# Kernel tuning notes

Measured on AMD Instinct MI355X. Metric: run time of the kernel, lower is better.

The kernel has to match this reference:

```python
import jax, jax.numpy as jnp
import numpy as np

N_NODES = 4096
N_EDGES = 16384
L = 512
MP_STEPS = 5
DT = 0.01


def _mlp(x, W1, b1, W2, b2):
    return jax.nn.relu(x @ W1 + b1) @ W2 + b2


def _ln(x):
    m = jnp.mean(x, axis=-1, keepdims=True)
    v = jnp.var(x, axis=-1, keepdims=True)
    return (x - m) * jax.lax.rsqrt(v + 1e-6)


_PARAM_SHAPES = [
    ("enc_e_W1", (1, L)), ("enc_e_b1", (L,)), ("enc_e_W2", (L, L)), ("enc_e_b2", (L,)),
    ("enc_n_W1", (1, L)), ("enc_n_b1", (L,)), ("enc_n_W2", (L, L)), ("enc_n_b2", (L,)),
    ("proc_e_W1", (3 * L, L)), ("proc_e_b1", (L,)), ("proc_e_W2", (L, L)), ("proc_e_b2", (L,)),
    ("proc_n_W1", (2 * L, L)), ("proc_n_b1", (L,)), ("proc_n_W2", (L, L)), ("proc_n_b2", (L,)),
    ("dec_e_W1", (L, L)), ("dec_e_b1", (L,)), ("dec_e_W2", (L, 1)), ("dec_e_b2", (1,)),
]


def setup_inputs() -> dict:
    key = jax.random.key(0)
    ks = jax.random.split(key, 3 + len(_PARAM_SHAPES))
    d = {}
    d["state"] = jax.random.normal(ks[0], (N_EDGES + N_NODES,), dtype=jnp.float32)
    d["senders"] = jax.random.randint(ks[1], (N_EDGES,), 0, N_NODES)
    d["receivers"] = jax.random.randint(ks[2], (N_EDGES,), 0, N_NODES)
    for i, (name, shp) in enumerate(_PARAM_SHAPES):
        if name.endswith(("b1", "b2")):
            d[name] = jnp.zeros(shp, dtype=jnp.float32)
        else:
            d[name] = 0.02 * jax.random.normal(ks[3 + i], shp, dtype=jnp.float32)
    return d


def _hamiltonian(x, senders, receivers,
                 enc_e_W1, enc_e_b1, enc_e_W2, enc_e_b2,
                 enc_n_W1, enc_n_b1, enc_n_W2, enc_n_b2,
                 proc_e_W1, proc_e_b1, proc_e_W2, proc_e_b2,
                 proc_n_W1, proc_n_b1, proc_n_W2, proc_n_b2,
                 dec_e_W1, dec_e_b1, dec_e_W2, dec_e_b2):
    # graph_from_state: edge scalars then node scalars
    e = x[:N_EDGES].reshape(N_EDGES, 1)
    n = x[N_EDGES:].reshape(N_NODES, 1)
    # encode (MLP + layer norm)
    eh = _ln(_mlp(e, enc_e_W1, enc_e_b1, enc_e_W2, enc_e_b2))  # [E, L]
    nh = _ln(_mlp(n, enc_n_W1, enc_n_b1, enc_n_W2, enc_n_b2))  # [N, L]
    # process: num_mp_steps of GraphNetwork-style message passing, shared params
    for _ in range(MP_STEPS):
        msg_in = jnp.concatenate([eh, nh[senders], nh[receivers]], axis=-1)  # [E, 3L]
        eh = eh + _mlp(msg_in, proc_e_W1, proc_e_b1, proc_e_W2, proc_e_b2)
        agg = jax.ops.segment_sum(eh, receivers, num_segments=N_NODES)  # [N, L]
        node_in = jnp.concatenate([nh, agg], axis=-1)  # [N, 2L]
        nh = nh + _mlp(node_in, proc_n_W1, proc_n_b1, proc_n_W2, proc_n_b2)
    # decode edges to scalars; H = sum of decoded edge energies
    dec_e = _mlp(eh, dec_e_W1, dec_e_b1, dec_e_W2, dec_e_b2)  # [E, 1]
    return jnp.sum(dec_e)


def reference(state, senders, receivers,
              enc_e_W1, enc_e_b1, enc_e_W2, enc_e_b2,
              enc_n_W1, enc_n_b1, enc_n_W2, enc_n_b2,
              proc_e_W1, proc_e_b1, proc_e_W2, proc_e_b2,
              proc_n_W1, proc_n_b1, proc_n_W2, proc_n_b2,
              dec_e_W1, dec_e_b1, dec_e_W2, dec_e_b2):
    def H_fn(x):
        return _hamiltonian(x, senders, receivers,
                            enc_e_W1, enc_e_b1, enc_e_W2, enc_e_b2,
                            enc_n_W1, enc_n_b1, enc_n_W2, enc_n_b2,
                            proc_e_W1, proc_e_b1, proc_e_W2, proc_e_b2,
                            proc_n_W1, proc_n_b1, proc_n_W2, proc_n_b2,
                            dec_e_W1, dec_e_b1, dec_e_W2, dec_e_b2)
    H, dH = jax.value_and_grad(H_fn)(state)
    # one integrator step driven by the Hamiltonian gradient (stand-in for DAE solve)
    next_state = state - DT * dH
    return next_state
```

## Files before the change

kernel.cpp:

```cpp
#include <hip/hip_runtime.h>


#define E_ROWS 16384
#define N_ROWS 4096
#define ALL_ROWS 20480
#define DT_F   0.01f

typedef unsigned char u8;
typedef unsigned short u16;
typedef unsigned long long u64;
typedef __attribute__((ext_vector_type(8))) short short8v;
typedef __attribute__((ext_vector_type(4))) float f32x4;

__device__ __forceinline__ u16 f2b(float f) {
    union { float f; unsigned u; } v; v.f = f;
    unsigned r = v.u + 0x7FFF + ((v.u >> 16) & 1);
    return (u16)(r >> 16);
}
__device__ __forceinline__ float b2f(u16 u) {
    union { unsigned u; float f; } v; v.u = ((unsigned)u) << 16;
    return v.f;
}

template<int BM, int WM, int WN, int KTOT, int LDA, int LDC,
         bool ADD_C, bool GATHER2, bool BIAS, bool RELU_MASK, bool APPLY_MASK,
         bool WF32, bool WBF16, bool DUALOUT, bool ROWDOT, bool DECW2, bool BSEL>
__global__ __launch_bounds__(256)
void bgemm(const u16* __restrict__ A, const u16* __restrict__ Bt, const u16* __restrict__ Bt2,
           float* __restrict__ C, u16* __restrict__ Cb,
           const u16* __restrict__ Cinb, const float* __restrict__ bias,
           const float* __restrict__ bias2, const u16* __restrict__ G12b,
           const int* __restrict__ sidx, const int* __restrict__ ridx,
           u8* __restrict__ maskw, u16* __restrict__ C2b,
           const float* __restrict__ wvec, const float* __restrict__ wvec2,
           float* __restrict__ outp)
{
    constexpr int BN = WN * 64;
    constexpr int NA = BM / 16;
    constexpr int TC = (BM + BN) / 16;
    constexpr int PER = TC / 4;
    constexpr int IFRAG = BM / WM / 16;
    __shared__ u16 Ls[BM * BN];

    const int tid = threadIdx.x;
    const int lane = tid & 63;
    const int wv = tid >> 6;
    const int wr = wv / WN;
    const int wc = wv % WN;

    const int gx = gridDim.x;
    int id = blockIdx.y * gx + blockIdx.x;
    const int nwg = gx * gridDim.y;
    id = (id & 7) * (nwg >> 3) + (id >> 3);
    const int bx = id % gx;
    const int by = id / gx;
    const int rowBase = by * BM;
    const int colBase = bx * BN;

    const u16* BtU = Bt;
    const float* biasU = bias;
    const float* wvecU = wvec;
    if (BSEL && rowBase >= E_ROWS) { BtU = Bt2; biasU = bias2; wvecU = wvec2; }

    const int srow = lane & 15;
    const int slotk = (lane >> 4) << 3;

    const u16* srcs[PER];
    int dstoff[PER];
#pragma unroll
    for (int q = 0; q < PER; ++q) {
        const int c = wv + (q << 2);
        if (c < NA)
            srcs[q] = A + (size_t)(rowBase + c * 16 + srow) * LDA + slotk;
        else
            srcs[q] = BtU + (size_t)(colBase + (c - NA) * 16 + srow) * KTOT + slotk;
        dstoff[q] = c * 512;
    }

    f32x4 acc[IFRAG][4];
#pragma unroll
    for (int i = 0; i < IFRAG; ++i)
#pragma unroll
        for (int j = 0; j < 4; ++j)
            acc[i][j] = (f32x4){0.f, 0.f, 0.f, 0.f};

    const int fro = ((lane >> 4) << 7) + ((lane & 15) << 3);

    for (int kb = 0; kb < KTOT; kb += 32) {
#pragma unroll
        for (int q = 0; q < PER; ++q)
            __builtin_amdgcn_global_load_lds(
                (const __attribute__((address_space(1))) void*)(srcs[q] + kb),
                (__attribute__((address_space(3))) void*)&Ls[dstoff[q]], 16, 0, 0);
        __syncthreads();
        short8v af[IFRAG], bfm[4];
#pragma unroll
        for (int i = 0; i < IFRAG; ++i)
            af[i] = *(const short8v*)&Ls[((wr * IFRAG + i) << 9) + fro];
#pragma unroll
        for (int j = 0; j < 4; ++j)
            bfm[j] = *(const short8v*)&Ls[((NA + (wc << 2) + j) << 9) + fro];
#pragma unroll
        for (int i = 0; i < IFRAG; ++i)
#pragma unroll
            for (int j = 0; j < 4; ++j)
                acc[i][j] = __builtin_amdgcn_mfma_f32_16x16x32_bf16(af[i], bfm[j], acc[i][j], 0, 0, 0);
        __syncthreads();
    }

    if constexpr (WF32) {
        const int colB = colBase + wc * 64 + (lane & 15);
        const int rowB = rowBase + wr * (BM / WM) + ((lane >> 4) << 2);
        float bcol[4];
#pragma unroll
        for (int j = 0; j < 4; ++j) bcol[j] = biasU[colB + (j << 4)];
#pragma unroll
        for (int i = 0; i < IFRAG; ++i)
#pragma unroll
            for (int r = 0; r < 4; ++r) {
                const int row = rowB + (i << 4) + r;
#pragma unroll
                for (int j = 0; j < 4; ++j)
                    C[(size_t)row * LDC + colB + (j << 4)] = acc[i][j][r] + bcol[j];
            }
    } else {
        const int colL = wc * 64 + (lane & 15);
        const int rowL0 = wr * (BM / WM) + ((lane >> 4) << 2);
#pragma unroll
        for (int i = 0; i < IFRAG; ++i)
#pragma unroll
            for (int r = 0; r < 4; ++r) {
                const int row = rowL0 + (i << 4) + r;
#pragma unroll
                for (int j = 0; j < 4; ++j) {
                    const int col = colL + (j << 4);
                    int byte = row * (BN * 2) + col * 2;
                    byte ^= (row & 7) << 4;
                    *(u16*)((char*)Ls + byte) = f2b(acc[i][j][r]);
                }
            }
        __syncthreads();

        constexpr int TPR = BN / 8;
        constexpr int RPP = 256 / TPR;
        constexpr int NP = BM / RPP;
        const int rloc = tid / TPR;
        const int seg = tid % TPR;
        const int col0 = seg * 8;
        const bool upper = DUALOUT && (colBase >= 512);
#pragma unroll
        for (int p = 0; p < NP; ++p) {
            const int row = p * RPP + rloc;
            const int grow = rowBase + row;
            const int gcol = colBase + col0;
            int byte = row * (BN * 2) + col0 * 2;
            byte ^= (row & 7) << 4;
            const short8v sv = *(const short8v*)((const char*)Ls + byte);
            float v[8];
#pragma unroll
            for (int e = 0; e < 8; ++e) v[e] = b2f((u16)sv[e]);

            if (DUALOUT && upper) {
                short8v res;
#pragma unroll
                for (int e = 0; e < 8; ++e) res[e] = (short)f2b(v[e]);
                *(short8v*)&C2b[(size_t)grow * 512 + (gcol - 512)] = res;
                continue;
            }
            if (GATHER2) {
                const int si = sidx[grow], ri = ridx[grow];
                const short8v g1 = *(const short8v*)&G12b[(size_t)si * 1024 + gcol];
                const short8v g2 = *(const short8v*)&G12b[(size_t)ri * 1024 + 512 + gcol];
#pragma unroll
                for (int e = 0; e < 8; ++e) v[e] += b2f((u16)g1[e]) + b2f((u16)g2[e]);
            }
            if (ADD_C) {
                const short8v c8 = *(const short8v*)&Cinb[(size_t)grow * LDC + gcol];
#pragma unroll
                for (int e = 0; e < 8; ++e) v[e] += b2f((u16)c8[e]);
            }
            if (BIAS) {
                const float4 b0 = *(const float4*)&biasU[gcol];
                const float4 b1 = *(const float4*)&biasU[gcol + 4];
                v[0] += b0.x; v[1] += b0.y; v[2] += b0.z; v[3] += b0.w;
                v[4] += b1.x; v[5] += b1.y; v[6] += b1.z; v[7] += b1.w;
            }
            if (DECW2) {
                const float4 w0 = *(const float4*)&wvecU[gcol];
                const float4 w1 = *(const float4*)&wvecU[gcol + 4];
                const float wl[8] = {w0.x, w0.y, w0.z, w0.w, w1.x, w1.y, w1.z, w1.w};
                short8v res;
#pragma unroll
                for (int e = 0; e < 8; ++e) res[e] = (v[e] > 0.f) ? (short)f2b(wl[e]) : (short)0;
                *(short8v*)&Cb[(size_t)grow * LDC + gcol] = res;
                continue;
            }
            if (RELU_MASK) {
                u64 mm = 0;
#pragma unroll
                for (int e = 0; e < 8; ++e) {
                    const bool m = v[e] > 0.f;
                    mm |= (u64)(m ? 1 : 0) << (e * 8);
                    if (!m) v[e] = 0.f;
                }
                *(u64*)&maskw[(size_t)grow * 512 + gcol] = mm;
            }
            if (APPLY_MASK) {
                const u64 mm = *(const u64*)&maskw[(size_t)grow * 512 + gcol];
#pragma unroll
                for (int e = 0; e < 8; ++e)
                    if (!((mm >> (e * 8)) & 0xff)) v[e] = 0.f;
            }
            if (ROWDOT) {
                const float4 w0 = *(const float4*)&wvecU[gcol];
                const float4 w1 = *(const float4*)&wvecU[gcol + 4];
                float rds = v[0] * w0.x + v[1] * w0.y + v[2] * w0.z + v[3] * w0.w
                          + v[4] * w1.x + v[5] * w1.y + v[6] * w1.z + v[7] * w1.w;
#pragma unroll
                for (int m = 1; m < TPR; m <<= 1) rds += __shfl_xor(rds, m);
                if (seg == 0) atomicAdd(outp + grow, -DT_F * rds);
            }
            if (WBF16) {
                short8v res;
#pragma unroll
                for (int e = 0; e < 8; ++e) res[e] = (short)f2b(v[e]);
                *(short8v*)&Cb[(size_t)grow * LDC + gcol] = res;
            }
        }
    }
}

struct WArgs {
    const float* src[10];
    u16* dstP[10];
    u16* dstT[10];
    int ldP[10], ldT[10];
};

__global__ void wcvt_kernel(WArgs a)
{
    const int i = blockIdx.z;
    const float* W = a.src[i];
    u16* P = a.dstP[i]; const int lp = a.ldP[i];
    u16* T = a.dstT[i]; const int lt = a.ldT[i];
    __shared__ u16 t[64][66];
    const int rb = blockIdx.y << 6, cb = blockIdx.x << 6;
    const int tr = threadIdx.x >> 4;
    const int tc = (threadIdx.x & 15) << 2;
#pragma unroll
    for (int rr = 0; rr < 4; ++rr) {
        const int r = tr + (rr << 4);
        const float4 v = *(const float4*)&W[(size_t)(rb + r) * 512 + cb + tc];
        ushort4 u; u.x = f2b(v.x); u.y = f2b(v.y); u.z = f2b(v.z); u.w = f2b(v.w);
        *(ushort4*)&P[(size_t)(rb + r) * lp + cb + tc] = u;
        t[r][tc] = u.x; t[r][tc + 1] = u.y; t[r][tc + 2] = u.z; t[r][tc + 3] = u.w;
    }
    __syncthreads();
#pragma unroll
    for (int rr = 0; rr < 4; ++rr) {
        const int n = tr + (rr << 4);
        ushort4 u;
        u.x = t[tc][n]; u.y = t[tc + 1][n]; u.z = t[tc + 2][n]; u.w = t[tc + 3][n];
        *(ushort4*)&T[(size_t)(cb + n) * lt + rb + tc] = u;
    }
}

__device__ void csr_build(const int* __restrict__ idx, int* __restrict__ starts,
                          int* __restrict__ eids)
{
    __shared__ int hist[4096];
    __shared__ int scanbuf[1024];
    const int t = threadIdx.x;
    for (int i = t; i < 4096; i += 1024) hist[i] = 0;
    __syncthreads();
    for (int e = t; e < 16384; e += 1024) atomicAdd(&hist[idx[e]], 1);
    __syncthreads();
    const int base = t << 2;
    const int l0 = hist[base], l1 = hist[base + 1], l2 = hist[base + 2], l3 = hist[base + 3];
    const int lsum = l0 + l1 + l2 + l3;
    scanbuf[t] = lsum;
    __syncthreads();
    for (int ofs = 1; ofs < 1024; ofs <<= 1) {
        const int v = scanbuf[t];
        const int u = (t >= ofs) ? scanbuf[t - ofs] : 0;
        __syncthreads();
        scanbuf[t] = v + u;
        __syncthreads();
    }
    const int excl = scanbuf[t] - lsum;
    const int p0 = excl, p1 = p0 + l0, p2 = p1 + l1, p3 = p2 + l2;
    starts[base] = p0; starts[base + 1] = p1; starts[base + 2] = p2; starts[base + 3] = p3;
    if (t == 0) starts[4096] = 16384;
    __syncthreads();
    hist[base] = p0; hist[base + 1] = p1; hist[base + 2] = p2; hist[base + 3] = p3;
    __syncthreads();
    for (int e = t; e < 16384; e += 1024) {
        const int pos = atomicAdd(&hist[idx[e]], 1);
        eids[pos] = e;
    }
    __syncthreads();
    for (int n = t; n < 4096; n += 1024) {
        const int s0 = starts[n], s1 = hist[n];
        for (int i = s0 + 1; i < s1; ++i) {
            const int v = eids[i];
            int j = i - 1;
            while (j >= s0 && eids[j] > v) { eids[j + 1] = eids[j]; --j; }
            eids[j + 1] = v;
        }
    }
}

__global__ __launch_bounds__(1024) void csr2_kernel(const int* __restrict__ senders,
                                                    const int* __restrict__ receivers,
                                                    int* __restrict__ sst, int* __restrict__ seid,
                                                    int* __restrict__ rst, int* __restrict__ reid)
{
    if (blockIdx.x == 0) csr_build(receivers, rst, reid);
    else                 csr_build(senders, sst, seid);
}

__global__ void init_out_kernel(const float* __restrict__ state, float* __restrict__ out)
{
    const int t = blockIdx.x * 256 + threadIdx.x;
    out[t] = state[t];
}

__global__ void seg_agg_fwd_kernel(const u16* __restrict__ ehb, const int* __restrict__ starts,
                                   const int* __restrict__ eids, const u16* __restrict__ nhb,
                                   u16* __restrict__ nagg)
{
    const int n = blockIdx.x, c = threadIdx.x;
    const int s0 = starts[n], s1 = starts[n + 1];
    float a0 = 0.f, a1 = 0.f;
    for (int i = s0; i < s1; ++i) {
        const u16* p = ehb + (size_t)eids[i] * 512;
        a0 += b2f(p[c]); a1 += b2f(p[c + 256]);
    }
    u16* d = nagg + (size_t)n * 1024;
    const u16* s = nhb + (size_t)n * 512;
    d[c] = s[c]; d[c + 256] = s[c + 256];
    d[512 + c] = f2b(a0); d[768 + c] = f2b(a1);
}

__global__ void seg_sr_bwd_kernel(const u16* __restrict__ dh1e,
                                  const int* __restrict__ sst, const int* __restrict__ seid,
                                  const int* __restrict__ rst, const int* __restrict__ reid,
                                  u16* __restrict__ SR)
{
    const int n = blockIdx.x, c = threadIdx.x;
    float a0 = 0.f, a1 = 0.f, b0 = 0.f, b1 = 0.f;
    for (int i = sst[n]; i < sst[n + 1]; ++i) {
        const u16* p = dh1e + (size_t)seid[i] * 512;
        a0 += b2f(p[c]); a1 += b2f(p[c + 256]);
    }
    for (int i = rst[n]; i < rst[n + 1]; ++i) {
        const u16* p = dh1e + (size_t)reid[i] * 512;
        b0 += b2f(p[c]); b1 += b2f(p[c + 256]);
    }
    u16* d = SR + (size_t)n * 1024;
    d[c] = f2b(a0); d[c + 256] = f2b(a1);
    d[512 + c] = f2b(b0); d[768 + c] = f2b(b1);
}

__global__ void enc_h1_kernel(const float* __restrict__ x,
                              const float* __restrict__ W1e, const float* __restrict__ b1e,
                              const float* __restrict__ W1n, const float* __restrict__ b1n,
                              u16* __restrict__ h1b, u8* __restrict__ mask)
{
    const int idx = blockIdx.x * 256 + threadIdx.x;
    const int row = idx >> 7;
    const int c = (idx & 127) << 2;
    const bool edge = row < E_ROWS;
    const float* W1 = edge ? W1e : W1n;
    const float* b1 = edge ? b1e : b1n;
    const float xv = x[row];
    const float4 w = *(const float4*)&W1[c];
    const float4 b = *(const float4*)&b1[c];
    float4 v;
    v.x = fmaf(xv, w.x, b.x); v.y = fmaf(xv, w.y, b.y);
    v.z = fmaf(xv, w.z, b.z); v.w = fmaf(xv, w.w, b.w);
    uchar4 m;
    m.x = v.x > 0.f; m.y = v.y > 0.f; m.z = v.z > 0.f; m.w = v.w > 0.f;
    v.x = m.x ? v.x : 0.f; v.y = m.y ? v.y : 0.f;
    v.z = m.z ? v.z : 0.f; v.w = m.w ? v.w : 0.f;
    const size_t o = (size_t)row * 512 + c;
    ushort4 u; u.x = f2b(v.x); u.y = f2b(v.y); u.z = f2b(v.z); u.w = f2b(v.w);
    *(ushort4*)&h1b[o] = u;
    *(uchar4*)&mask[o] = m;
}

__global__ void ln_fwd_kernel(const float* __restrict__ x, u16* __restrict__ xhat_b,
                              u16* __restrict__ xb, float* __restrict__ rstd_save)
{
    const int row = blockIdx.x, tid = threadIdx.x;
    const float* p = x + (size_t)row * 512;
    const float a = p[tid], b = p[tid + 256];
    __shared__ float s1[256], s2[256];
    s1[tid] = a + b; s2[tid] = a * a + b * b;
    __syncthreads();
    for (int d = 128; d > 0; d >>= 1) {
        if (tid < d) { s1[tid] += s1[tid + d]; s2[tid] += s2[tid + d]; }
        __syncthreads();
    }
    const float mean = s1[0] * (1.f / 512.f);
    const float var = s2[0] * (1.f / 512.f) - mean * mean;
    const float r = rsqrtf(var + 1e-6f);
    const float ya = (a - mean) * r, yb = (b - mean) * r;
    const size_t o = (size_t)row * 512 + tid;
    xhat_b[o] = f2b(ya); xhat_b[o + 256] = f2b(yb);
    xb[o] = f2b(ya); xb[o + 256] = f2b(yb);
    if (tid == 0) rstd_save[row] = r;
}

__global__ void ln_bwd_kernel(u16* __restrict__ d, const u16* __restrict__ xhat_b,
                              const float* __restrict__ rstd)
{
    const int row = blockIdx.x, tid = threadIdx.x;
    u16* p = d + (size_t)row * 512;
    const u16* xh = xhat_b + (size_t)row * 512;
    const float da = b2f(p[tid]), dbv = b2f(p[tid + 256]);
    const float xa = b2f(xh[tid]), xbv = b2f(xh[tid + 256]);
    __shared__ float s1[256], s2[256];
    s1[tid] = da + dbv; s2[tid] = da * xa + dbv * xbv;
    __syncthreads();
    for (int dd = 128; dd > 0; dd >>= 1) {
        if (tid < dd) { s1[tid] += s1[tid + dd]; s2[tid] += s2[tid + dd]; }
        __syncthreads();
    }
    const float m1 = s1[0] * (1.f / 512.f);
    const float m2 = s2[0] * (1.f / 512.f);
    const float r = rstd[row];
    p[tid] = f2b(r * (da - m1 - xa * m2));
    p[tid + 256] = f2b(r * (dbv - m1 - xbv * m2));
}

__global__ void gather_add_kernel(u16* __restrict__ dst, const u16* __restrict__ src,
                                  const int* __restrict__ idx)
{
    const int t = blockIdx.x * 256 + threadIdx.x;
    const int row = t >> 6;
    const int c = (t & 63) << 3;
    const size_t o = (size_t)row * 512 + c;
    short8v a = *(const short8v*)&dst[o];
    const short8v g = *(const short8v*)&src[(size_t)idx[row] * 512 + c];
    short8v r;
#pragma unroll
    for (int i = 0; i < 8; ++i)
        r[i] = (short)f2b(b2f((u16)a[i]) + b2f((u16)g[i]));
    *(short8v*)&dst[o] = r;
}

extern "C" void kernel_launch(void* const* d_in, const int* in_sizes, int n_in,
                              void* d_out, int out_size, void* d_ws, size_t ws_size,
                              hipStream_t stream)
{
    (void)in_sizes; (void)n_in; (void)out_size; (void)ws_size;
    const float* state     = (const float*)d_in[0];
    const int*   senders   = (const int*)d_in[1];
    const int*   receivers = (const int*)d_in[2];
    const float* enc_e_W1 = (const float*)d_in[3];
    const float* enc_e_b1 = (const float*)d_in[4];
    const float* enc_e_W2 = (const float*)d_in[5];
    const float* enc_e_b2 = (const float*)d_in[6];
    const float* enc_n_W1 = (const float*)d_in[7];
    const float* enc_n_b1 = (const float*)d_in[8];
    const float* enc_n_W2 = (const float*)d_in[9];
    const float* enc_n_b2 = (const float*)d_in[10];
    const float* pe_W1 = (const float*)d_in[11];
    const float* pe_b1 = (const float*)d_in[12];
    const float* pe_W2 = (const float*)d_in[13];
    const float* pe_b2 = (const float*)d_in[14];
    const float* pn_W1 = (const float*)d_in[15];
    const float* pn_b1 = (const float*)d_in[16];
    const float* pn_W2 = (const float*)d_in[17];
    const float* pn_b2 = (const float*)d_in[18];
    const float* de_W1 = (const float*)d_in[19];
    const float* de_b1 = (const float*)d_in[20];
    const float* de_W2 = (const float*)d_in[21];
    float* out = (float*)d_out;

    const size_t EL = (size_t)E_ROWS * 512, NL = (size_t)N_ROWS * 512;
    const size_t AL = (size_t)ALL_ROWS * 512;
    const size_t LL = 512 * 512;
    char* w = (char*)d_ws;
    size_t off = 0;
    auto carve = [&](size_t bytes) -> char* {
        char* p = w + off;
        off += (bytes + 255) & ~(size_t)255;
        return p;
    };
    u16* wb = (u16*)carve(20 * LL * 2);
    u16* WT0 = wb;           u16* WT1 = wb + LL;      u16* WT2 = wb + 2 * LL;
    u16* WT34 = wb + 3 * LL;                          u16* WT5 = wb + 5 * LL;
    u16* WT8 = wb + 6 * LL;  u16* WT9 = wb + 7 * LL;
    u16* WP0 = wb + 8 * LL;  u16* WP1 = wb + 9 * LL;  u16* WP2 = wb + 10 * LL;
    u16* WP5 = wb + 11 * LL; u16* WP8 = wb + 12 * LL; u16* WP9 = wb + 13 * LL;
    u16* WT67 = wb + 14 * LL;
    u16* WP34c = wb + 16 * LL;
    u16* WP67 = wb + 18 * LL;

    float* eh  = (float*)carve(AL * 4);
    u16* ehb   = (u16*)carve(EL * 2);
    u16* nhb   = (u16*)carve(NL * 2);
    u16* h1eb  = (u16*)carve(EL * 2);
    u16* h1nb  = (u16*)carve(NL * 2);
    u16* eh0b  = (u16*)carve(EL * 2);
    u16* nh0b  = (u16*)carve(NL * 2);
    u8* menc   = (u8*)carve(AL);
    u16* G1b   = (u16*)carve(NL * 2);
    u16* G12b  = (u16*)carve(NL * 2 * 2);
    u16* nsr   = (u16*)carve(NL * 2 * 2);
    float* rstd = (float*)carve(ALL_ROWS * 4);
    u8* mpe    = (u8*)carve(5 * EL);
    u8* mpn    = (u8*)carve(5 * NL);
    int* rst  = (int*)carve(4097 * 4);
    int* reid = (int*)carve(16384 * 4);
    int* sst  = (int*)carve(4097 * 4);
    int* seid = (int*)carve(16384 * 4);

    const dim3 blk(256);
    const dim3 gE(4, E_ROWS / 128);
    const dim3 gA(4, ALL_ROWS / 128);
    const dim3 gN512(8, N_ROWS / 64);
    const dim3 gN1024(16, N_ROWS / 64);
    const float* fp = nullptr;
    u16* up = nullptr;
    const u16* cup = nullptr;
    const int* ip = nullptr;
    u8* mp = nullptr;
    float* f2p = nullptr;

    WArgs wa;
    const float* wsrc[10] = { enc_e_W2, enc_n_W2, pe_W1, pe_W1 + LL, pe_W1 + 2 * LL,
                              pe_W2, pn_W1, pn_W1 + LL, pn_W2, de_W1 };
    u16* dstP[10] = { WP0, WP1, WP2, WP34c, WP34c + 512, WP5, WP67, WP67 + LL, WP8, WP9 };
    int  ldP [10] = { 512, 512, 512, 1024,  1024,        512, 512,  512,       512, 512 };
    u16* dstT[10] = { WT0, WT1, WT2, WT34, WT34 + LL, WT5, WT67, WT67 + 512, WT8, WT9 };
    int  ldT [10] = { 512, 512, 512, 512,  512,       512, 1024, 1024,       512, 512 };
    for (int i = 0; i < 10; ++i) {
        wa.src[i] = wsrc[i]; wa.dstP[i] = dstP[i]; wa.dstT[i] = dstT[i];
        wa.ldP[i] = ldP[i]; wa.ldT[i] = ldT[i];
    }
    wcvt_kernel<<<dim3(8, 8, 10), blk, 0, stream>>>(wa);

    csr2_kernel<<<2, 1024, 0, stream>>>(senders, receivers, sst, seid, rst, reid);
    init_out_kernel<<<ALL_ROWS / 256, blk, 0, stream>>>(state, out);

    enc_h1_kernel<<<ALL_ROWS * 128 / 256, blk, 0, stream>>>(state, enc_e_W1, enc_e_b1,
                                                            enc_n_W1, enc_n_b1, h1eb, menc);
    bgemm<128,2,2,512,512,512, false,false,true,false,false, true,false,false,false,false,true>
        <<<gA, blk, 0, stream>>>(h1eb, WT0, WT1, eh, up, cup, enc_e_b2, enc_n_b2, cup, ip, ip, mp, up, fp, fp, f2p);
    ln_fwd_kernel<<<ALL_ROWS, blk, 0, stream>>>(eh, eh0b, ehb, rstd);

    for (int k = 0; k < 5; ++k) {
        bgemm<64,4,1,512,512,1024, false,false,false,false,false, false,true,false,false,false,false>
            <<<gN1024, blk, 0, stream>>>(nhb, WT34, cup, f2p, G12b, cup, fp, fp, cup, ip, ip, mp, up, fp, fp, f2p);
        bgemm<128,2,2,512,512,512, false,true,true,true,false, false,true,false,false,false,false>
            <<<gE, blk, 0, stream>>>(ehb, WT2, cup, f2p, h1eb, cup, pe_b1, fp, G12b, senders, receivers, mpe + (size_t)k * EL, up, fp, fp, f2p);
        bgemm<128,2,2,512,512,512, true,false,true,false,false, false,true,false,false,false,false>
            <<<gE, blk, 0, stream>>>(h1eb, WT5, cup, f2p, ehb, ehb, pe_b2, fp, cup, ip, ip, mp, up, fp, fp, f2p);
        seg_agg_fwd_kernel<<<N_ROWS, blk, 0, stream>>>(ehb, rst, reid, nhb, nsr);
        bgemm<64,4,1,1024,1024,512, false,false,true,true,false, false,true,false,false,false,false>
            <<<gN512, blk, 0, stream>>>(nsr, WT67, cup, f2p, h1nb, cup, pn_b1, fp, cup, ip, ip, mpn + (size_t)k * NL, up, fp, fp, f2p);
        bgemm<64,4,1,512,512,512, true,false,true,false,false, false,true,false,false,false,false>
            <<<gN512, blk, 0, stream>>>(h1nb, WT8, cup, f2p, nhb, nhb, pn_b2, fp, cup, ip, ip, mp, up, fp, fp, f2p);
    }

    bgemm<128,2,2,512,512,512, false,false,true,false,false, false,false,false,false,true,false>
        <<<gE, blk, 0, stream>>>(ehb, WT9, cup, f2p, h1eb, cup, de_b1, fp, cup, ip, ip, mp, up, de_W2, fp, f2p);

    bgemm<128,2,2,512,512,512, false,false,false,false,false, false,true,false,false,false,false>
        <<<gE, blk, 0, stream>>>(h1eb, WP9, cup, f2p, ehb, cup, fp, fp, cup, ip, ip, mp, up, fp, fp, f2p);

    for (int k = 4; k >= 0; --k) {
        if (k < 4) {
            bgemm<64,4,1,512,512,512, false,false,false,false,true, false,true,false,false,false,false>
                <<<gN512, blk, 0, stream>>>(nhb, WP8, cup, f2p, h1nb, cup, fp, fp, cup, ip, ip, mpn + (size_t)k * NL, up, fp, fp, f2p);
            bgemm<64,4,1,512,512,512, true,false,false,false,false, false,true,true,false,false,false>
                <<<gN1024, blk, 0, stream>>>(h1nb, WP67, cup, f2p, nhb, nhb, fp, fp, cup, ip, ip, mp, G1b, fp, fp, f2p);
            gather_add_kernel<<<E_ROWS * 64 / 256, blk, 0, stream>>>(ehb, G1b, receivers);
        }
        bgemm<128,2,2,512,512,512, false,false,false,false,true, false,true,false,false,false,false>
            <<<gE, blk, 0, stream>>>(ehb, WP5, cup, f2p, h1eb, cup, fp, fp, cup, ip, ip, mpe + (size_t)k * EL, up, fp, fp, f2p);
        bgemm<128,2,2,512,512,512, true,false,false,false,false, false,true,false,false,false,false>
            <<<gE, blk, 0, stream>>>(h1eb, WP2, cup, f2p, ehb, ehb, fp, fp, cup, ip, ip, mp, up, fp, fp, f2p);
        seg_sr_bwd_kernel<<<N_ROWS, blk, 0, stream>>>(h1eb, sst, seid, rst, reid, nsr);
        if (k == 4)
            bgemm<64,4,1,1024,1024,512, false,false,false,false,false, false,true,false,false,false,false>
                <<<gN512, blk, 0, stream>>>(nsr, WP34c, cup, f2p, nhb, cup, fp, fp, cup, ip, ip, mp, up, fp, fp, f2p);
        else
            bgemm<64,4,1,1024,1024,512, true,false,false,false,false, false,true,false,false,false,false>
                <<<gN512, blk, 0, stream>>>(nsr, WP34c, cup, f2p, nhb, nhb, fp, fp, cup, ip, ip, mp, up, fp, fp, f2p);
    }

    ln_bwd_kernel<<<ALL_ROWS, blk, 0, stream>>>(ehb, eh0b, rstd);
    bgemm<128,2,2,512,512,512, false,false,false,false,true, false,false,false,true,false,true>
        <<<gA, blk, 0, stream>>>(ehb, WP0, WP1, f2p, up, cup, fp, fp, cup, ip, ip, menc, up, enc_e_W1, enc_n_W1, out);
}
```

Before: 1.261 ms.

## Fuse back-to-back edge MLP GEMMs into one kernel keeping hidden tile in LDS

Adds an mlp2 kernel that computes both layers of the edge MLP for a 64-row tile in one launch. The 64x512 hidden activation stays in swizzled LDS instead of going through HBM, and the weight tiles are double-buffered. It replaces the paired edge GEMMs in the forward message-passing step, the decoder forward plus its backward, and the backward edge MLP, removing the h1 HBM round trip and a launch per pair. In exchange each block holds a full row tile and recomputes nothing, but it uses large LDS (about 96KB), which limits occupancy, and the grid is only 256 blocks.

```diff
diff --git a/kernel.cpp b/kernel.cpp
--- a/kernel.cpp
+++ b/kernel.cpp
@@ -21,10 +21,261 @@
     union { unsigned u; float f; } v; v.u = ((unsigned)u) << 16;
     return v.f;
 }
+__device__ __forceinline__ void gld16(const u16* g, u16* l) {
+    __builtin_amdgcn_global_load_lds((const __attribute__((address_space(1))) void*)g,
+                                     (__attribute__((address_space(3))) void*)l, 16, 0, 0);
+}
+
+template<int MODE>
+__global__ __launch_bounds__(512)
+void mlp2(const u16* __restrict__ A, const u16* __restrict__ B1t,
+          const u16* __restrict__ B2t,
+          const float* __restrict__ bias1, const float* __restrict__ bias2,
+          const u16* __restrict__ G12b,
+          const int* __restrict__ sidx, const int* __restrict__ ridx,
+          u8* __restrict__ maskio, u16* __restrict__ h1hbm,
+          u16* __restrict__ Cout, const float* __restrict__ w2vec)
+{
+    __shared__ u16 Hs[64 * 512];
+    __shared__ u16 Bs[2][32 * 512];
+    char* HsB = (char*)Hs;
+
+    const int tid = threadIdx.x;
+    const int lane = tid & 63;
+    const int wv = tid >> 6;
+    const int wr = wv >> 2;
+    const int wc = wv & 3;
+
+    int id = blockIdx.x;
+    id = (id & 7) * (gridDim.x >> 3) + (id >> 3);
+    const int rowBase = id * 64;
+
+    const int srow = lane & 15;
+    const int slotk = (lane >> 4) << 3;
+    const int fro = ((lane >> 4) << 7) + ((lane & 15) << 3);
+
+    f32x4 acc[2][8];
+#pragma unroll
+    for (int i = 0; i < 2; ++i)
+#pragma unroll
+        for (int j = 0; j < 8; ++j)
+            acc[i][j] = (f32x4){0.f, 0.f, 0.f, 0.f};
+
+    auto stage1 = [&](int buf, int kb) {
+#pragma unroll
+        for (int q = 0; q < 5; ++q) {
+            const int c = wv + (q << 3);
+            if (c >= 36) continue;
+            if (c < 4)
+                gld16(A + (size_t)(rowBase + c * 16 + srow) * 512 + kb + slotk,
+                      Hs + buf * 2048 + c * 512);
+            else
+                gld16(B1t + (size_t)((c - 4) * 16 + srow) * 512 + kb + slotk,
+                      &Bs[buf][(c - 4) * 512]);
+        }
+    };
+    stage1(0, 0);
+    asm volatile("s_waitcnt vmcnt(0)" ::: "memory");
+    __builtin_amdgcn_s_barrier();
+    asm volatile("" ::: "memory");
+#pragma unroll
+    for (int t = 0; t < 16; ++t) {
+        const int cur = t & 1;
+        if (t < 15) stage1(cur ^ 1, (t + 1) * 32);
+        const u16* AsC = Hs + cur * 2048;
+        short8v af[2], bf[8];
+#pragma unroll
+        for (int i = 0; i < 2; ++i)
+            af[i] = *(const short8v*)&AsC[((wr << 1) + i) * 512 + fro];
+#pragma unroll
+        for (int j = 0; j < 8; ++j)
+            bf[j] = *(const short8v*)&Bs[cur][((wc << 3) + j) * 512 + fro];
+#pragma unroll
+        for (int i = 0; i < 2; ++i)
+#pragma unroll
+            for (int j = 0; j < 8; ++j)
+                acc[i][j] = __builtin_amdgcn_mfma_f32_16x16x32_bf16(af[i], bf[j], acc[i][j], 0, 0, 0);
+        if (t < 15) {
+            asm volatile("s_waitcnt vmcnt(0)" ::: "memory");
+            __builtin_amdgcn_s_barrier();
+            asm volatile("" ::: "memory");
+        }
+    }
+    __syncthreads();
+
+#pragma unroll
+    for (int i = 0; i < 2; ++i)
+#pragma unroll
+        for (int r = 0; r < 4; ++r) {
+            const int drow = wr * 32 + i * 16 + ((lane >> 4) << 2) + r;
+#pragma unroll
+            for (int j = 0; j < 8; ++j) {
+                const int dcol = wc * 128 + j * 16 + (lane & 15);
+                int db = drow * 1024 + dcol * 2;
+                db ^= (drow & 7) << 4;
+                *(u16*)(HsB + db) = f2b(acc[i][j][r]);
+            }
+        }
+    __syncthreads();
+
+    {
+        const int rloc = tid >> 6;
+        const int seg = tid & 63;
+        const int col0 = seg << 3;
+#pragma unroll
+        for (int p = 0; p < 8; ++p) {
+            const int row = p * 8 + rloc;
+            const int grow = rowBase + row;
+            int byte = row * 1024 + col0 * 2;
+            byte ^= (row & 7) << 4;
+            const short8v sv = *(const short8v*)(HsB + byte);
+            float v[8];
+#pragma unroll
+            for (int e = 0; e < 8; ++e) v[e] = b2f((u16)sv[e]);
+
+            if (MODE == 0) {
+                const int si = sidx[grow], ri = ridx[grow];
+                const short8v g1 = *(const short8v*)&G12b[(size_t)si * 1024 + col0];
+                const short8v g2 = *(const short8v*)&G12b[(size_t)ri * 1024 + 512 + col0];
+                const float4 b0 = *(const float4*)&bias1[col0];
+                const float4 b1v = *(const float4*)&bias1[col0 + 4];
+                const float bl[8] = {b0.x, b0.y, b0.z, b0.w, b1v.x, b1v.y, b1v.z, b1v.w};
+#pragma unroll
+                for (int e = 0; e < 8; ++e) v[e] += b2f((u16)g1[e]) + b2f((u16)g2[e]) + bl[e];
+                u64 mm = 0;
+#pragma unroll
+                for (int e = 0; e < 8; ++e) {
+                    const bool m = v[e] > 0.f;
+                    mm |= (u64)(m ? 1 : 0) << (e * 8);
+                    if (!m) v[e] = 0.f;
+                }
+                *(u64*)&maskio[(size_t)grow * 512 + col0] = mm;
+                short8v h;
+#pragma unroll
+                for (int e = 0; e < 8; ++e) h[e] = (short)f2b(v[e]);
+                *(short8v*)(HsB + byte) = h;
+            } else if (MODE == 1) {
+                const u64 mm = *(const u64*)&maskio[(size_t)grow * 512 + col0];
+                short8v h;
+#pragma unroll
+                for (int e = 0; e < 8; ++e) {
+                    if (!((mm >> (e * 8)) & 0xff)) v[e] = 0.f;
+                    h[e] = (short)f2b(v[e]);
+                }
+                *(short8v*)&h1hbm[(size_t)grow * 512 + col0] = h;
+                *(short8v*)(HsB + byte) = h;
+            } else {
+                const float4 b0 = *(const float4*)&bias1[col0];
+                const float4 b1v = *(const float4*)&bias1[col0 + 4];
+                const float4 w0 = *(const float4*)&w2vec[col0];
+                const float4 w1 = *(const float4*)&w2vec[col0 + 4];
+                const float bl[8] = {b0.x, b0.y, b0.z, b0.w, b1v.x, b1v.y, b1v.z, b1v.w};
+                const float wl[8] = {w0.x, w0.y, w0.z, w0.w, w1.x, w1.y, w1.z, w1.w};
+                short8v h;
+#pragma unroll
+                for (int e = 0; e < 8; ++e)
+                    h[e] = (v[e] + bl[e] > 0.f) ? (short)f2b(wl[e]) : (short)0;
+                *(short8v*)(HsB + byte) = h;
+            }
+        }
+    }
+    __syncthreads();
+
+#pragma unroll
+    for (int i = 0; i < 2; ++i)
+#pragma unroll
+        for (int j = 0; j < 8; ++j)
+            acc[i][j] = (f32x4){0.f, 0.f, 0.f, 0.f};
+
+    auto stage2 = [&](int buf, int kb) {
+#pragma unroll
+        for (int q = 0; q < 4; ++q) {
+            const int c = wv + (q << 3);
+            gld16(B2t + (size_t)(c * 16 + srow) * 512 + kb + slotk, &Bs[buf][c * 512]);
+        }
+    };
+    stage2(0, 0);
+    __syncthreads();
+#pragma unroll
+    for (int t = 0; t < 16; ++t) {
+        const int cur = t & 1;
+        if (t < 15) stage2(cur ^ 1, (t + 1) * 32);
+        short8v af[2], bf[8];
+#pragma unroll
+        for (int i = 0; i < 2; ++i) {
+            const int arow = wr * 32 + i * 16 + (lane & 15);
+            int ab = arow * 1024 + t * 64 + ((lane >> 4) << 4);
+            ab ^= (arow & 7) << 4;
+            af[i] = *(const short8v*)(HsB + ab);
+        }
+#pragma unroll
+        for (int j = 0; j < 8; ++j)
+            bf[j] = *(const short8v*)&Bs[cur][((wc << 3) + j) * 512 + fro];
+#pragma unroll
+        for (int i = 0; i < 2; ++i)
+#pragma unroll
+            for (int j = 0; j < 8; ++j)
+                acc[i][j] = __builtin_amdgcn_mfma_f32_16x16x32_bf16(af[i], bf[j], acc[i][j], 0, 0, 0);
+        if (t < 15) {
+            asm volatile("s_waitcnt vmcnt(0)" ::: "memory");
+            __builtin_amdgcn_s_barrier();
+            asm volatile("" ::: "memory");
+        }
+    }
+    __syncthreads();
+
+#pragma unroll
+    for (int i = 0; i < 2; ++i)
+#pragma unroll
+        for (int r = 0; r < 4; ++r) {
+            const int drow = wr * 32 + i * 16 + ((lane >> 4) << 2) + r;
+#pragma unroll
+            for (int j = 0; j < 8; ++j) {
+                const int dcol = wc * 128 + j * 16 + (lane & 15);
+                int db = drow * 1024 + dcol * 2;
+                db ^= (drow & 7) << 4;
+                *(u16*)(HsB + db) = f2b(acc[i][j][r]);
+            }
+        }
+    __syncthreads();
+
+    {
+        const int rloc = tid >> 6;
+        const int seg = tid & 63;
+        const int col0 = seg << 3;
+#pragma unroll
+        for (int p = 0; p < 8; ++p) {
+            const int row = p * 8 + rloc;
+            const int grow = rowBase + row;
+            int byte = row * 1024 + col0 * 2;
+            byte ^= (row & 7) << 4;
+            const short8v sv = *(const short8v*)(HsB + byte);
+            float v[8];
+#pragma unroll
+            for (int e = 0; e < 8; ++e) v[e] = b2f((u16)sv[e]);
+            if (MODE == 0 || MODE == 1) {
+                const short8v c8 = *(const short8v*)&Cout[(size_t)grow * 512 + col0];
+#pragma unroll
+                for (int e = 0; e < 8; ++e) v[e] += b2f((u16)c8[e]);
+            }
+            if (MODE == 0) {
+                const float4 b0 = *(const float4*)&bias2[col0];
+                const float4 b1v = *(const float4*)&bias2[col0 + 4];
+                const float bl[8] = {b0.x, b0.y, b0.z, b0.w, b1v.x, b1v.y, b1v.z, b1v.w};
+#pragma unroll
+                for (int e = 0; e < 8; ++e) v[e] += bl[e];
+            }
+            short8v res;
+#pragma unroll
+            for (int e = 0; e < 8; ++e) res[e] = (short)f2b(v[e]);
+            *(short8v*)&Cout[(size_t)grow * 512 + col0] = res;
+        }
+    }
+}
 
 template<int BM, int WM, int WN, int KTOT, int LDA, int LDC,
          bool ADD_C, bool GATHER2, bool BIAS, bool RELU_MASK, bool APPLY_MASK,
-         bool WF32, bool WBF16, bool DUALOUT, bool ROWDOT, bool DECW2, bool BSEL>
+         bool WF32, bool WBF16, bool DUALOUT, bool ROWDOT, bool BSEL>
 __global__ __launch_bounds__(256)
 void bgemm(const u16* __restrict__ A, const u16* __restrict__ Bt, const u16* __restrict__ Bt2,
            float* __restrict__ C, u16* __restrict__ Cb,
@@ -89,9 +340,7 @@
     for (int kb = 0; kb < KTOT; kb += 32) {
 #pragma unroll
         for (int q = 0; q < PER; ++q)
-            __builtin_amdgcn_global_load_lds(
-                (const __attribute__((address_space(1))) void*)(srcs[q] + kb),
-                (__attribute__((address_space(3))) void*)&Ls[dstoff[q]], 16, 0, 0);
+            gld16(srcs[q] + kb, &Ls[dstoff[q]]);
         __syncthreads();
         short8v af[IFRAG], bfm[4];
 #pragma unroll
@@ -184,16 +433,6 @@
                 const float4 b1 = *(const float4*)&biasU[gcol + 4];
                 v[0] += b0.x; v[1] += b0.y; v[2] += b0.z; v[3] += b0.w;
                 v[4] += b1.x; v[5] += b1.y; v[6] += b1.z; v[7] += b1.w;
-            }
-            if (DECW2) {
-                const float4 w0 = *(const float4*)&wvecU[gcol];
-                const float4 w1 = *(const float4*)&wvecU[gcol + 4];
-                const float wl[8] = {w0.x, w0.y, w0.z, w0.w, w1.x, w1.y, w1.z, w1.w};
-                short8v res;
-#pragma unroll
-                for (int e = 0; e < 8; ++e) res[e] = (v[e] > 0.f) ? (short)f2b(wl[e]) : (short)0;
-                *(short8v*)&Cb[(size_t)grow * LDC + gcol] = res;
-                continue;
             }
             if (RELU_MASK) {
                 u64 mm = 0;
@@ -519,7 +758,8 @@
     int* seid = (int*)carve(16384 * 4);
 
     const dim3 blk(256);
-    const dim3 gE(4, E_ROWS / 128);
+    const dim3 blk512(512);
+    const dim3 gF(E_ROWS / 64);
     const dim3 gA(4, ALL_ROWS / 128);
     const dim3 gN512(8, N_ROWS / 64);
     const dim3 gN1024(16, N_ROWS / 64);
@@ -548,52 +788,44 @@
 
     enc_h1_kernel<<<ALL_ROWS * 128 / 256, blk, 0, stream>>>(state, enc_e_W1, enc_e_b1,
                                                             enc_n_W1, enc_n_b1, h1eb, menc);
-    bgemm<128,2,2,512,512,512, false,false,true,false,false, true,false,false,false,false,true>
+    bgemm<128,2,2,512,512,512, false,false,true,false,false, true,false,false,false,true>
         <<<gA, blk, 0, stream>>>(h1eb, WT0, WT1, eh, up, cup, enc_e_b2, enc_n_b2, cup, ip, ip, mp, up, fp, fp, f2p);
     ln_fwd_kernel<<<ALL_ROWS, blk, 0, stream>>>(eh, eh0b, ehb, rstd);
 
     for (int k = 0; k < 5; ++k) {
-        bgemm<64,4,1,512,512,1024, false,false,false,false,false, false,true,false,false,false,false>
+        bgemm<64,4,1,512,512,1024, false,false,false,false,false, false,true,false,false,false>
             <<<gN1024, blk, 0, stream>>>(nhb, WT34, cup, f2p, G12b, cup, fp, fp, cup, ip, ip, mp, up, fp, fp, f2p);
-        bgemm<128,2,2,512,512,512, false,true,true,true,false, false,true,false,false,false,false>
-            <<<gE, blk, 0, stream>>>(ehb, WT2, cup, f2p, h1eb, cup, pe_b1, fp, G12b, senders, receivers, mpe + (size_t)k * EL, up, fp, fp, f2p);
-        bgemm<128,2,2,512,512,512, true,false,true,false,false, false,true,false,false,false,false>
-            <<<gE, blk, 0, stream>>>(h1eb, WT5, cup, f2p, ehb, ehb, pe_b2, fp, cup, ip, ip, mp, up, fp, fp, f2p);
+        mlp2<0><<<gF, blk512, 0, stream>>>(ehb, WT2, WT5, pe_b1, pe_b2, G12b,
+                                           senders, receivers, mpe + (size_t)k * EL, up, ehb, fp);
         seg_agg_fwd_kernel<<<N_ROWS, blk, 0, stream>>>(ehb, rst, reid, nhb, nsr);
-        bgemm<64,4,1,1024,1024,512, false,false,true,true,false, false,true,false,false,false,false>
+        bgemm<64,4,1,1024,1024,512, false,false,true,true,false, false,true,false,false,false>
             <<<gN512, blk, 0, stream>>>(nsr, WT67, cup, f2p, h1nb, cup, pn_b1, fp, cup, ip, ip, mpn + (size_t)k * NL, up, fp, fp, f2p);
-        bgemm<64,4,1,512,512,512, true,false,true,false,false, false,true,false,false,false,false>
+        bgemm<64,4,1,512,512,512, true,false,true,false,false, false,true,false,false,false>
             <<<gN512, blk, 0, stream>>>(h1nb, WT8, cup, f2p, nhb, nhb, pn_b2, fp, cup, ip, ip, mp, up, fp, fp, f2p);
     }
 
-    bgemm<128,2,2,512,512,512, false,false,true,false,false, false,false,false,false,true,false>
-        <<<gE, blk, 0, stream>>>(ehb, WT9, cup, f2p, h1eb, cup, de_b1, fp, cup, ip, ip, mp, up, de_W2, fp, f2p);
-
-    bgemm<128,2,2,512,512,512, false,false,false,false,false, false,true,false,false,false,false>
-        <<<gE, blk, 0, stream>>>(h1eb, WP9, cup, f2p, ehb, cup, fp, fp, cup, ip, ip, mp, up, fp, fp, f2p);
+    mlp2<2><<<gF, blk512, 0, stream>>>(ehb, WT9, WP9, de_b1, fp, cup, ip, ip, mp, up, ehb, de_W2);
 
     for (int k = 4; k >= 0; --k) {
         if (k < 4) {
-            bgemm<64,4,1,512,512,512, false,false,false,false,true, false,true,false,false,false,false>
+            bgemm<64,4,1,512,512,512, false,false,false,false,true, false,true,false,false,false>
                 <<<gN512, blk, 0, stream>>>(nhb, WP8, cup, f2p, h1nb, cup, fp, fp, cup, ip, ip, mpn + (size_t)k * NL, up, fp, fp, f2p);
-            bgemm<64,4,1,512,512,512, true,false,false,false,false, false,true,true,false,false,false>
+            bgemm<64,4,1,512,512,512, true,false,false,false,false, false,true,true,false,false>
                 <<<gN1024, blk, 0, stream>>>(h1nb, WP67, cup, f2p, nhb, nhb, fp, fp, cup, ip, ip, mp, G1b, fp, fp, f2p);
             gather_add_kernel<<<E_ROWS * 64 / 256, blk, 0, stream>>>(ehb, G1b, receivers);
         }
-        bgemm<128,2,2,512,512,512, false,false,false,false,true, false,true,false,false,false,false>
-            <<<gE, blk, 0, stream>>>(ehb, WP5, cup, f2p, h1eb, cup, fp, fp, cup, ip, ip, mpe + (size_t)k * EL, up, fp, fp, f2p);
-        bgemm<128,2,2,512,512,512, true,false,false,false,false, false,true,false,false,false,false>
-            <<<gE, blk, 0, stream>>>(h1eb, WP2, cup, f2p, ehb, ehb, fp, fp, cup, ip, ip, mp, up, fp, fp, f2p);
+        mlp2<1><<<gF, blk512, 0, stream>>>(ehb, WP5, WP2, fp, fp, cup, ip, ip,
+                                           mpe + (size_t)k * EL, h1eb, ehb, fp);
         seg_sr_bwd_kernel<<<N_ROWS, blk, 0, stream>>>(h1eb, sst, seid, rst, reid, nsr);
         if (k == 4)
-            bgemm<64,4,1,1024,1024,512, false,false,false,false,false, false,true,false,false,false,false>
+            bgemm<64,4,1,1024,1024,512, false,false,false,false,false, false,true,false,false,false>
                 <<<gN512, blk, 0, stream>>>(nsr, WP34c, cup, f2p, nhb, cup, fp, fp, cup, ip, ip, mp, up, fp, fp, f2p);
         else
-            bgemm<64,4,1,1024,1024,512, true,false,false,false,false, false,true,false,false,false,false>
+            bgemm<64,4,1,1024,1024,512, true,false,false,false,false, false,true,false,false,false>
                 <<<gN512, blk, 0, stream>>>(nsr, WP34c, cup, f2p, nhb, nhb, fp, fp, cup, ip, ip, mp, up, fp, fp, f2p);
     }
 
     ln_bwd_kernel<<<ALL_ROWS, blk, 0, stream>>>(ehb, eh0b, rstd);
-    bgemm<128,2,2,512,512,512, false,false,false,false,true, false,false,false,true,false,true>
+    bgemm<128,2,2,512,512,512, false,false,false,false,true, false,false,false,true,true>
         <<<gA, blk, 0, stream>>>(ehb, WP0, WP1, f2p, up, cup, fp, fp, cup, ip, ip, menc, up, enc_e_W1, enc_n_W1, out);
 }
```

Result: slower. 1.315 ms (+4.3%).

## Triple-buffer LDS tiles in bgemm with async prefetch two stages ahead

Applied to the files above, without the earlier changes.

Replaces the single-buffer load-sync-compute-sync loop with a three-stage LDS ring. Global-to-LDS loads for tile t+2 are issued before computing tile t. Partial vmcnt waits plus a single barrier per iteration replace the two full syncs. This hides global memory latency behind MFMA work, at the cost of more shared memory per block, which may lower occupancy.

```diff
diff --git a/kernel.cpp b/kernel.cpp
--- a/kernel.cpp
+++ b/kernel.cpp
@@ -20,6 +20,16 @@
 __device__ __forceinline__ float b2f(u16 u) {
     union { unsigned u; float f; } v; v.u = ((unsigned)u) << 16;
     return v.f;
+}
+__device__ __forceinline__ void gld16(const u16* g, u16* l) {
+    __builtin_amdgcn_global_load_lds((const __attribute__((address_space(1))) void*)g,
+                                     (__attribute__((address_space(3))) void*)l, 16, 0, 0);
+}
+template<int N> __device__ __forceinline__ void waitcnt_vm() {
+    if constexpr (N == 0)      asm volatile("s_waitcnt vmcnt(0)" ::: "memory");
+    else if constexpr (N == 2) asm volatile("s_waitcnt vmcnt(2)" ::: "memory");
+    else if constexpr (N == 4) asm volatile("s_waitcnt vmcnt(4)" ::: "memory");
+    else if constexpr (N == 8) asm volatile("s_waitcnt vmcnt(8)" ::: "memory");
 }
 
 template<int BM, int WM, int WN, int KTOT, int LDA, int LDC,
@@ -39,8 +49,11 @@
     constexpr int NA = BM / 16;
     constexpr int TC = (BM + BN) / 16;
     constexpr int PER = TC / 4;
+    constexpr int NT = KTOT / 32;
     constexpr int IFRAG = BM / WM / 16;
-    __shared__ u16 Ls[BM * BN];
+    constexpr int BUFU = TC * 512;
+    constexpr int LSZ = (3 * BUFU > BM * BN) ? 3 * BUFU : BM * BN;
+    __shared__ u16 Ls[LSZ];
 
     const int tid = threadIdx.x;
     const int lane = tid & 63;
@@ -86,27 +99,43 @@
 
     const int fro = ((lane >> 4) << 7) + ((lane & 15) << 3);
 
-    for (int kb = 0; kb < KTOT; kb += 32) {
-#pragma unroll
-        for (int q = 0; q < PER; ++q)
-            __builtin_amdgcn_global_load_lds(
-                (const __attribute__((address_space(1))) void*)(srcs[q] + kb),
-                (__attribute__((address_space(3))) void*)&Ls[dstoff[q]], 16, 0, 0);
-        __syncthreads();
+#pragma unroll
+    for (int q = 0; q < PER; ++q) gld16(srcs[q], &Ls[dstoff[q]]);
+#pragma unroll
+    for (int q = 0; q < PER; ++q) gld16(srcs[q] + 32, &Ls[BUFU + dstoff[q]]);
+    waitcnt_vm<PER>();
+    __builtin_amdgcn_s_barrier();
+    asm volatile("" ::: "memory");
+
+    for (int t = 0; t < NT; ++t) {
+        const int cur = t % 3;
+        if (t + 2 < NT) {
+            const int nxt = (t + 2) % 3;
+#pragma unroll
+            for (int q = 0; q < PER; ++q)
+                gld16(srcs[q] + (t + 2) * 32, &Ls[nxt * BUFU + dstoff[q]]);
+        }
+        const u16* Lc = &Ls[cur * BUFU];
         short8v af[IFRAG], bfm[4];
 #pragma unroll
         for (int i = 0; i < IFRAG; ++i)
-            af[i] = *(const short8v*)&Ls[((wr * IFRAG + i) << 9) + fro];
+            af[i] = *(const short8v*)&Lc[((wr * IFRAG + i) << 9) + fro];
 #pragma unroll
         for (int j = 0; j < 4; ++j)
-            bfm[j] = *(const short8v*)&Ls[((NA + (wc << 2) + j) << 9) + fro];
+            bfm[j] = *(const short8v*)&Lc[((NA + (wc << 2) + j) << 9) + fro];
 #pragma unroll
         for (int i = 0; i < IFRAG; ++i)
 #pragma unroll
             for (int j = 0; j < 4; ++j)
                 acc[i][j] = __builtin_amdgcn_mfma_f32_16x16x32_bf16(af[i], bfm[j], acc[i][j], 0, 0, 0);
-        __syncthreads();
-    }
+        if (t + 1 < NT) {
+            if (t + 2 < NT) waitcnt_vm<PER>();
+            else            waitcnt_vm<0>();
+            __builtin_amdgcn_s_barrier();
+            asm volatile("" ::: "memory");
+        }
+    }
+    __syncthreads();
 
     if constexpr (WF32) {
         const int colB = colBase + wc * 64 + (lane & 15);
```

After: 1.237 ms. Within noise of the previous version (-1.9%).
